# Kernel tuning notes

Hardware: AMD Instinct MI355X
Metric: run time of the kernel (lower is better)

## Reference

```python
import jax, jax.numpy as jnp
import numpy as np

G = 2000      # num_genes
TF = 64       # num_tf
B = 32        # batch (cells)
_peaks = 5 + (np.arange(G) % 46)          # ragged peaks per gene, avg ~27
T = int(_peaks.sum())                      # 54736 total peak columns
E = G * 16                                 # directed edges before symmetrization


def setup_inputs() -> dict:
    key = jax.random.key(0)
    ks = jax.random.split(key, 8)
    x = jax.random.normal(ks[0], (B, TF, T), jnp.float32)
    # gene id of each peak column (sorted, ragged segment structure = cut[])
    gene_ids = jnp.asarray(np.repeat(np.arange(G), _peaks), jnp.int32)
    # all per-gene subNet Linear weights flattened into one [TF, T] table
    w_sub = jax.random.normal(ks[1], (TF, T), jnp.float32) * 0.02
    b_sub = jax.random.normal(ks[2], (G,), jnp.float32) * 0.02
    rng = np.random.default_rng(1)
    src = rng.integers(0, G, E)
    dst = rng.integers(0, G, E)
    ei = np.stack([np.concatenate([src, dst]), np.concatenate([dst, src])])
    edge_index = jnp.asarray(ei, jnp.int32)                 # [2, 2E], symmetrized
    w_conv = jax.random.normal(ks[3], (1, 2), jnp.float32) * 0.5   # GCN lin weight (in=1, out=2)
    b_conv = jax.random.normal(ks[4], (2,), jnp.float32) * 0.1
    w_out = jax.random.normal(ks[5], (G * 2, 3), jnp.float32) * 0.02
    b_out = jax.random.normal(ks[6], (3,), jnp.float32) * 0.02
    return dict(x=x, gene_ids=gene_ids, w_sub=w_sub, b_sub=b_sub,
                edge_index=edge_index, w_conv=w_conv, b_conv=b_conv,
                w_out=w_out, b_out=b_out)


def reference(x, gene_ids, w_sub, b_sub, edge_index, w_conv, b_conv, w_out, b_out):
    # --- ragged per-gene subNets: Linear(num_peak_i*TF, 1) each ---
    # out[b,g] = sum_{t, p in gene g} x[b,t,p] * w[g,t,p] + b_sub[g]
    z = (x * w_sub[None]).sum(axis=1)                        # [B, T] reduce over TF
    x_cat = jnp.zeros((x.shape[0], b_sub.shape[0]), x.dtype)
    x_cat = x_cat.at[:, gene_ids].add(z) + b_sub[None]       # segment-sum over peaks
    x_cat = jax.nn.relu(x_cat)                               # cat_activate

    # --- GCNConv(1, 2, add_self_loops=False) on node features [B, G, 1] ---
    h = jnp.einsum('bn,f->bnf', x_cat, w_conv[0])            # lin: [B, G, 2]
    src, dst = edge_index[0], edge_index[1]
    deg = jnp.zeros((b_sub.shape[0],), x.dtype).at[dst].add(1.0)
    dinv = jnp.where(deg > 0, jax.lax.rsqrt(jnp.maximum(deg, 1.0)), 0.0)
    norm = dinv[src] * dinv[dst]                             # [2E]
    msg = h[:, src, :] * norm[None, :, None]                 # gather + scale
    agg = jnp.zeros_like(h).at[:, dst, :].add(msg) + b_conv  # scatter-add + bias
    g = jax.nn.relu(agg).reshape(x.shape[0], -1)             # [B, G*2]

    out = g @ w_out + b_out                                   # [B, 3]
    return x_cat, g, out
```

## Files before the change

### kernel.cpp

```cpp
#include <hip/hip_runtime.h>


typedef float f32x4 __attribute__((ext_vector_type(4)));

__global__ void k_subnet(const float* __restrict__ x, const float* __restrict__ w_sub,
                         const int* __restrict__ gene_ids, float* __restrict__ acc,
                         int TF, int T, int G) {
    int t = (blockIdx.x * blockDim.x + threadIdx.x) * 4;
    int b = blockIdx.y;
    if (t >= T) return;
    const size_t xbase = (size_t)b * TF * T;
    if (t + 3 < T && (T % 4) == 0) {
        const f32x4* xp = (const f32x4*)(x + xbase + t);
        const f32x4* wp = (const f32x4*)(w_sub + t);
        const size_t strideV = (size_t)T / 4;
        f32x4 a = {0.f, 0.f, 0.f, 0.f};
        #pragma unroll 8
        for (int tf = 0; tf < TF; ++tf) {
            f32x4 xv = __builtin_nontemporal_load(xp + (size_t)tf * strideV);
            f32x4 wv = wp[(size_t)tf * strideV];
            a += xv * wv;
        }
        int4 gi = *(const int4*)(gene_ids + t);
        float* base = acc + (size_t)b * G;
        float v = a.x; int cg = gi.x;
        if (gi.y == cg) v += a.y; else { atomicAdd(base + cg, v); cg = gi.y; v = a.y; }
        if (gi.z == cg) v += a.z; else { atomicAdd(base + cg, v); cg = gi.z; v = a.z; }
        if (gi.w == cg) v += a.w; else { atomicAdd(base + cg, v); cg = gi.w; v = a.w; }
        atomicAdd(base + cg, v);
    } else {
        for (int tt = t; tt < T && tt < t + 4; ++tt) {
            float a = 0.f;
            for (int tf = 0; tf < TF; ++tf)
                a += x[xbase + (size_t)tf * T + tt] * w_sub[(size_t)tf * T + tt];
            atomicAdd(acc + (size_t)b * G + gene_ids[tt], a);
        }
    }
}

__global__ void k_xcatdeg(const float* __restrict__ acc, const float* __restrict__ b_sub,
                          float* __restrict__ xcat,
                          const int* __restrict__ ei, float* __restrict__ deg,
                          const float* __restrict__ b_out, float* __restrict__ out_fin,
                          int BG, int G, int E2, int B3) {
    int i = blockIdx.x * blockDim.x + threadIdx.x;
    if (i < BG) {
        int g = i % G;
        float v = acc[i] + b_sub[g];
        xcat[i] = v > 0.f ? v : 0.f;
    }
    if (i < E2) atomicAdd(&deg[ei[E2 + i]], 1.0f);
    if (i < B3) out_fin[i] = b_out[i % 3];
}

__global__ void k_scatter(const float* __restrict__ xcat, const int* __restrict__ ei,
                          const float* __restrict__ deg, float* __restrict__ s,
                          int G, int E2) {
    int e = blockIdx.x * blockDim.x + threadIdx.x;
    if (e >= E2) return;
    int b = blockIdx.y;
    int src = ei[e], dst = ei[E2 + e];
    float ds = deg[src], dd = deg[dst];
    float ns = (ds > 0.f) ? (1.0f / sqrtf(fmaxf(ds, 1.0f))) : 0.f;
    float nd = (dd > 0.f) ? (1.0f / sqrtf(fmaxf(dd, 1.0f))) : 0.f;
    atomicAdd(&s[(size_t)b * G + dst], xcat[(size_t)b * G + src] * (ns * nd));
}

__global__ void k_gfinout(const float* __restrict__ s, const float* __restrict__ w_conv,
                          const float* __restrict__ b_conv, const float* __restrict__ w_out,
                          float* __restrict__ gout, float* __restrict__ out_fin, int G) {
    int n = blockIdx.x * blockDim.x + threadIdx.x;
    int b = blockIdx.y;
    float a0 = 0.f, a1 = 0.f, a2 = 0.f;
    if (n < G) {
        size_t i = (size_t)b * G + n;
        float sv = s[i];
        float g0 = sv * w_conv[0] + b_conv[0]; g0 = g0 > 0.f ? g0 : 0.f;
        float g1 = sv * w_conv[1] + b_conv[1]; g1 = g1 > 0.f ? g1 : 0.f;
        gout[2 * i + 0] = g0;
        gout[2 * i + 1] = g1;
        const float* w0 = w_out + (size_t)6 * n;
        a0 = g0 * w0[0] + g1 * w0[3];
        a1 = g0 * w0[1] + g1 * w0[4];
        a2 = g0 * w0[2] + g1 * w0[5];
    }
    for (int off = 32; off > 0; off >>= 1) {
        a0 += __shfl_down(a0, off);
        a1 += __shfl_down(a1, off);
        a2 += __shfl_down(a2, off);
    }
    __shared__ float red[3][4];
    int lane = threadIdx.x & 63;
    int wid  = threadIdx.x >> 6;
    if (lane == 0) { red[0][wid] = a0; red[1][wid] = a1; red[2][wid] = a2; }
    __syncthreads();
    if (threadIdx.x == 0) {
        atomicAdd(&out_fin[b * 3 + 0], red[0][0] + red[0][1] + red[0][2] + red[0][3]);
        atomicAdd(&out_fin[b * 3 + 1], red[1][0] + red[1][1] + red[1][2] + red[1][3]);
        atomicAdd(&out_fin[b * 3 + 2], red[2][0] + red[2][1] + red[2][2] + red[2][3]);
    }
}

extern "C" void kernel_launch(void* const* d_in, const int* in_sizes, int n_in,
                              void* d_out, int out_size, void* d_ws, size_t ws_size,
                              hipStream_t stream) {
    const float* x        = (const float*)d_in[0];
    const int*   gene_ids = (const int*)d_in[1];
    const float* w_sub    = (const float*)d_in[2];
    const float* b_sub    = (const float*)d_in[3];
    const int*   ei       = (const int*)d_in[4];
    const float* w_conv   = (const float*)d_in[5];
    const float* b_conv   = (const float*)d_in[6];
    const float* w_out    = (const float*)d_in[7];
    const float* b_out    = (const float*)d_in[8];

    const int G  = in_sizes[3];
    const int T  = in_sizes[1];
    const int TF = in_sizes[2] / T;
    const int B  = in_sizes[0] / (TF * T);
    const int E2 = in_sizes[4] / 2;
    const int BG = B * G;

    float* acc = (float*)d_ws;
    float* deg = acc + BG;
    float* s   = deg + G;
    hipMemsetAsync(d_ws, 0, (size_t)(BG + G + BG) * sizeof(float), stream);

    float* out_xcat = (float*)d_out;
    float* out_g    = out_xcat + BG;
    float* out_fin  = out_g + (size_t)2 * BG;

    {
        int tthreads = (T + 3) / 4;
        dim3 grid((tthreads + 255) / 256, B);
        k_subnet<<<grid, 256, 0, stream>>>(x, w_sub, gene_ids, acc, TF, T, G);
    }
    {
        int mx = BG > E2 ? BG : E2;
        int b3 = B * 3;
        if (mx < b3) mx = b3;
        k_xcatdeg<<<(mx + 255) / 256, 256, 0, stream>>>(acc, b_sub, out_xcat, ei, deg,
                                                        b_out, out_fin, BG, G, E2, b3);
    }
    {
        dim3 grid((E2 + 255) / 256, B);
        k_scatter<<<grid, 256, 0, stream>>>(out_xcat, ei, deg, s, G, E2);
    }
    {
        dim3 grid((G + 255) / 256, B);
        k_gfinout<<<grid, 256, 0, stream>>>(s, w_conv, b_conv, w_out, out_g, out_fin, G);
    }
}
```

Before: 722.5 us.

## Fuse all stages into one cooperative persistent kernel with grid syncs

After: 1.121 ms. 55.2% more time.

```diff
diff --git a/kernel.cpp b/kernel.cpp
--- a/kernel.cpp
+++ b/kernel.cpp
@@ -1,7 +1,115 @@
 #include <hip/hip_runtime.h>
+#include <hip/hip_cooperative_groups.h>
+
+namespace cg = cooperative_groups;
 
 
 typedef float f32x4 __attribute__((ext_vector_type(4)));
+
+__global__ __launch_bounds__(256, 4)
+void k_mega(const float* __restrict__ x, const int* __restrict__ gene_ids,
+            const float* __restrict__ w_sub, const float* __restrict__ b_sub,
+            const int* __restrict__ ei, const float* __restrict__ w_conv,
+            const float* __restrict__ b_conv, const float* __restrict__ w_out,
+            const float* __restrict__ b_out,
+            float* __restrict__ acc, float* __restrict__ deg, float* __restrict__ s,
+            float* __restrict__ out_xcat, float* __restrict__ out_g,
+            float* __restrict__ out_fin,
+            int B, int TF, int T, int G, int E2) {
+    cg::grid_group gg = cg::this_grid();
+    const int tid = blockIdx.x * blockDim.x + threadIdx.x;
+    const int nth = gridDim.x * blockDim.x;
+    const int BG = B * G;
+
+    const int ztot = BG + G + BG;
+    for (int i = tid; i < ztot; i += nth) acc[i] = 0.f;
+    if (tid < B * 3) out_fin[tid] = b_out[tid % 3];
+    gg.sync();
+
+    {
+        const int NQ = T >> 2;
+        const int njobs = B * NQ;
+        const size_t strideV = (size_t)NQ;
+        for (int job = tid; job < njobs; job += nth) {
+            int b = job / NQ;
+            int q = job - b * NQ;
+            int t = q << 2;
+            const f32x4* xp = (const f32x4*)(x + (size_t)b * TF * T + t);
+            const f32x4* wp = (const f32x4*)(w_sub + t);
+            f32x4 a = {0.f, 0.f, 0.f, 0.f};
+            #pragma unroll 8
+            for (int tf = 0; tf < TF; ++tf) {
+                f32x4 xv = __builtin_nontemporal_load(xp + (size_t)tf * strideV);
+                f32x4 wv = wp[(size_t)tf * strideV];
+                a += xv * wv;
+            }
+            int4 gi = *(const int4*)(gene_ids + t);
+            float* base = acc + (size_t)b * G;
+            float v = a.x; int cgid = gi.x;
+            if (gi.y == cgid) v += a.y; else { atomicAdd(base + cgid, v); cgid = gi.y; v = a.y; }
+            if (gi.z == cgid) v += a.z; else { atomicAdd(base + cgid, v); cgid = gi.z; v = a.z; }
+            if (gi.w == cgid) v += a.w; else { atomicAdd(base + cgid, v); cgid = gi.w; v = a.w; }
+            atomicAdd(base + cgid, v);
+        }
+    }
+    gg.sync();
+
+    for (int i = tid; i < BG; i += nth) {
+        int g = i % G;
+        float v = acc[i] + b_sub[g];
+        out_xcat[i] = v > 0.f ? v : 0.f;
+    }
+    for (int e = tid; e < E2; e += nth) atomicAdd(&deg[ei[E2 + e]], 1.0f);
+    gg.sync();
+
+    {
+        const int etot = B * E2;
+        for (int idx = tid; idx < etot; idx += nth) {
+            int b = idx / E2;
+            int e = idx - b * E2;
+            int src = ei[e], dst = ei[E2 + e];
+            float ds = deg[src], dd = deg[dst];
+            float ns = (ds > 0.f) ? (1.0f / sqrtf(fmaxf(ds, 1.0f))) : 0.f;
+            float nd = (dd > 0.f) ? (1.0f / sqrtf(fmaxf(dd, 1.0f))) : 0.f;
+            atomicAdd(&s[(size_t)b * G + dst], out_xcat[(size_t)b * G + src] * (ns * nd));
+        }
+    }
+    gg.sync();
+
+    {
+        const float wc0 = w_conv[0], wc1 = w_conv[1];
+        const float bc0 = b_conv[0], bc1 = b_conv[1];
+        const int wid = tid >> 6, lane = tid & 63;
+        const int WPB = (G + 63) >> 6;
+        if (wid < B * WPB) {
+            int b = wid / WPB;
+            int n = (wid - b * WPB) * 64 + lane;
+            float a0 = 0.f, a1 = 0.f, a2 = 0.f;
+            if (n < G) {
+                size_t i = (size_t)b * G + n;
+                float sv = s[i];
+                float g0 = fmaxf(sv * wc0 + bc0, 0.f);
+                float g1 = fmaxf(sv * wc1 + bc1, 0.f);
+                out_g[2 * i + 0] = g0;
+                out_g[2 * i + 1] = g1;
+                const float* w0 = w_out + (size_t)6 * n;
+                a0 = g0 * w0[0] + g1 * w0[3];
+                a1 = g0 * w0[1] + g1 * w0[4];
+                a2 = g0 * w0[2] + g1 * w0[5];
+            }
+            for (int off = 32; off > 0; off >>= 1) {
+                a0 += __shfl_down(a0, off);
+                a1 += __shfl_down(a1, off);
+                a2 += __shfl_down(a2, off);
+            }
+            if (lane == 0) {
+                atomicAdd(&out_fin[b * 3 + 0], a0);
+                atomicAdd(&out_fin[b * 3 + 1], a1);
+                atomicAdd(&out_fin[b * 3 + 2], a2);
+            }
+        }
+    }
+}
 
 __global__ void k_subnet(const float* __restrict__ x, const float* __restrict__ w_sub,
                          const int* __restrict__ gene_ids, float* __restrict__ acc,
@@ -23,11 +131,11 @@
         }
         int4 gi = *(const int4*)(gene_ids + t);
         float* base = acc + (size_t)b * G;
-        float v = a.x; int cg = gi.x;
-        if (gi.y == cg) v += a.y; else { atomicAdd(base + cg, v); cg = gi.y; v = a.y; }
-        if (gi.z == cg) v += a.z; else { atomicAdd(base + cg, v); cg = gi.z; v = a.z; }
-        if (gi.w == cg) v += a.w; else { atomicAdd(base + cg, v); cg = gi.w; v = a.w; }
-        atomicAdd(base + cg, v);
+        float v = a.x; int cgid = gi.x;
+        if (gi.y == cgid) v += a.y; else { atomicAdd(base + cgid, v); cgid = gi.y; v = a.y; }
+        if (gi.z == cgid) v += a.z; else { atomicAdd(base + cgid, v); cgid = gi.z; v = a.z; }
+        if (gi.w == cgid) v += a.w; else { atomicAdd(base + cgid, v); cgid = gi.w; v = a.w; }
+        atomicAdd(base + cgid, v);
     } else {
         for (int tt = t; tt < T && tt < t + 4; ++tt) {
             float a = 0.f;
@@ -114,22 +222,33 @@
     const float* w_out    = (const float*)d_in[7];
     const float* b_out    = (const float*)d_in[8];
 
-    const int G  = in_sizes[3];
-    const int T  = in_sizes[1];
-    const int TF = in_sizes[2] / T;
-    const int B  = in_sizes[0] / (TF * T);
-    const int E2 = in_sizes[4] / 2;
+    int G  = in_sizes[3];
+    int T  = in_sizes[1];
+    int TF = in_sizes[2] / T;
+    int B  = in_sizes[0] / (TF * T);
+    int E2 = in_sizes[4] / 2;
     const int BG = B * G;
 
     float* acc = (float*)d_ws;
     float* deg = acc + BG;
     float* s   = deg + G;
-    hipMemsetAsync(d_ws, 0, (size_t)(BG + G + BG) * sizeof(float), stream);
 
     float* out_xcat = (float*)d_out;
     float* out_g    = out_xcat + BG;
     float* out_fin  = out_g + (size_t)2 * BG;
 
+    void* args[] = {
+        (void*)&x, (void*)&gene_ids, (void*)&w_sub, (void*)&b_sub, (void*)&ei,
+        (void*)&w_conv, (void*)&b_conv, (void*)&w_out, (void*)&b_out,
+        (void*)&acc, (void*)&deg, (void*)&s,
+        (void*)&out_xcat, (void*)&out_g, (void*)&out_fin,
+        (void*)&B, (void*)&TF, (void*)&T, (void*)&G, (void*)&E2
+    };
+    hipError_t err = hipLaunchCooperativeKernel((const void*)k_mega, dim3(1024), dim3(256),
+                                                args, 0, stream);
+    if (err == hipSuccess) return;
+
+    hipMemsetAsync(d_ws, 0, (size_t)(BG + G + BG) * sizeof(float), stream);
     {
         int tthreads = (T + 3) / 4;
         dim3 grid((tthreads + 255) / 256, B);
```
